# Kernel tuning notes

Hardware: AMD Instinct MI355X
Metric: run time of the kernel (lower is better)

Reference implementation:

```python
import jax, jax.numpy as jnp
import numpy as np

B, S, E, H = 4, 2048, 1024, 16
D = E // H  # head_size = 64


def setup_inputs() -> dict:
    key = jax.random.key(0)
    k1, k2 = jax.random.split(key)
    x = jax.random.normal(k1, (B, S, E), dtype=jnp.float32)
    # fused QKV projection weight (torch Linear(E, 3E, bias=False))
    W_qkv = jax.random.normal(k2, (E, 3 * E), dtype=jnp.float32) * (1.0 / np.sqrt(E))
    return {"x": x, "W_qkv": W_qkv}


def reference(x, W_qkv):
    b, s, e = x.shape
    qkv = x @ W_qkv                              # [B,S,3E]
    q, k, v = jnp.split(qkv, 3, axis=-1)
    # [B,S,E] -> [B,H,S,D]
    q = q.reshape(b, s, H, D).transpose(0, 2, 1, 3)
    k = k.reshape(b, s, H, D).transpose(0, 2, 1, 3)
    v = v.reshape(b, s, H, D).transpose(0, 2, 1, 3)
    scores = jnp.einsum("bhqd,bhkd->bhqk", q, k) * (1.0 / np.sqrt(D))
    causal = jnp.tril(jnp.ones((s, s), dtype=bool))  # [S,S]
    scores = jnp.where(causal[None, None, :, :], scores, jnp.float32(-jnp.inf))
    attn = jax.nn.softmax(scores, axis=-1)
    # dropout is identity in eval mode (p effectively 0 for this baseline)
    out = jnp.einsum("bhqk,bhkd->bhqd", attn, v)  # [B,H,S,D]
    out = out.transpose(0, 2, 1, 3).reshape(b, s, e)
    # NOTE: original forward never applies output_projection; faithful omission.
    return out
```

## Files before the change

kernel.cpp:

```cpp
#include <hip/hip_runtime.h>
#include <hip/hip_bf16.h>
#include <cstdint>
#include <cstddef>

#define GLOBAL_AS __attribute__((address_space(1)))
#define LDS_AS __attribute__((address_space(3)))

typedef short bf16x8 __attribute__((ext_vector_type(8)));
typedef float f32x4 __attribute__((ext_vector_type(4)));

constexpr int Bq = 4, Sq = 2048, Eq = 1024, Hh = 16;
constexpr int M = Bq * Sq;
constexpr int K = 1024;
constexpr int N = 3 * Eq;

#define SMSC 0.18033688f
#define SMBIAS (-16.0f)

#if __has_builtin(__builtin_amdgcn_exp2f)
#define EXP2F(x) __builtin_amdgcn_exp2f(x)
#else
#define EXP2F(x) exp2f(x)
#endif

static __device__ __forceinline__ unsigned f2bf(float f) {
    union { float f; unsigned u; } v; v.f = f;
    unsigned r = v.u + 0x7fffu + ((v.u >> 16) & 1u);
    return r >> 16;
}

static __device__ __forceinline__ unsigned pk2(float a, float b) {
    union { __hip_bfloat162 h; unsigned u; } c;
    c.h = __float22bfloat162_rn(float2{a, b});
    return c.u;
}

static __device__ __forceinline__ void pl32swap(unsigned& a, unsigned& b) {
    asm("v_permlane32_swap_b32 %0, %1" : "+v"(a), "+v"(b));
}
static __device__ __forceinline__ void pl16swap(unsigned& a, unsigned& b) {
    asm("v_permlane16_swap_b32 %0, %1" : "+v"(a), "+v"(b));
}

__global__ __launch_bounds__(256) void prep(const float* __restrict__ X,
                                            unsigned short* __restrict__ Xb,
                                            const float* __restrict__ W,
                                            unsigned short* __restrict__ Wt) {
    __shared__ unsigned short tile[64 * 72];
    const int t = threadIdx.x;
    const int bx = blockIdx.x;
    if (bx < 4096) {
        size_t i = ((size_t)bx * 256 + t) * 8;
        float4 a = *reinterpret_cast<const float4*>(X + i);
        float4 b = *reinterpret_cast<const float4*>(X + i + 4);
        uint4 o;
        o.x = pk2(a.x, a.y);
        o.y = pk2(a.z, a.w);
        o.z = pk2(b.x, b.y);
        o.w = pk2(b.z, b.w);
        *reinterpret_cast<uint4*>(Xb + i) = o;
        return;
    }
    const int idx = bx - 4096;
    const int n0 = (idx % 48) * 64;
    const int k0 = (idx / 48) * 64;
    #pragma unroll
    for (int p = 0; p < 4; ++p) {
        int c = p * 256 + t;
        int row = c >> 4;
        int c4 = (c & 15) * 4;
        float4 v = *reinterpret_cast<const float4*>(W + (size_t)(k0 + row) * N + n0 + c4);
        *reinterpret_cast<unsigned*>(&tile[row * 72 + c4]) = pk2(v.x, v.y);
        *reinterpret_cast<unsigned*>(&tile[row * 72 + c4 + 2]) = pk2(v.z, v.w);
    }
    __syncthreads();
    #pragma unroll
    for (int p = 0; p < 2; ++p) {
        int c = t + p * 256;
        int n = c & 63;
        int kc = (c >> 6) * 8;
        unsigned v[8];
        #pragma unroll
        for (int j = 0; j < 8; ++j) v[j] = tile[(kc + j) * 72 + n];
        uint4 o;
        o.x = v[0] | (v[1] << 16);
        o.y = v[2] | (v[3] << 16);
        o.z = v[4] | (v[5] << 16);
        o.w = v[6] | (v[7] << 16);
        *reinterpret_cast<uint4*>(Wt + (size_t)(n0 + n) * K + k0 + kc) = o;
    }
}

__global__ __launch_bounds__(512) void gemm_qkv(const unsigned short* __restrict__ A,
                                                const unsigned short* __restrict__ Bt,
                                                unsigned short* __restrict__ C,
                                                unsigned short* __restrict__ Vt) {
    __shared__ unsigned short Al[3][256 * 64];
    __shared__ unsigned short Bl[3][128 * 64];
    const int t = threadIdx.x;
    const int lane = t & 63, w = t >> 6;
    const int wm = w >> 1, wn = w & 1;
    const int lr = lane & 15, quad = lane >> 4;
    const int swz = lr & 7;

    const int bid = (int)blockIdx.x;
    const int sid = (bid & 7) * 96 + (bid >> 3);
    const int nb = sid % 24, mb = sid / 24;
    const int m0 = mb * 256, n0 = nb * 128;

    auto stA = [&](int kt, int s, int p) {
        int c = p * 512 + t;
        int row = c >> 3;
        int lch = (c & 7) ^ (row & 7);
        const unsigned short* g = A + (size_t)(m0 + row) * K + kt * 64 + lch * 8;
        __builtin_amdgcn_global_load_lds((const GLOBAL_AS unsigned int*)g,
                                         (LDS_AS unsigned int*)&Al[s][c * 8], 16, 0, 0);
    };
    auto stB = [&](int kt, int s, int p) {
        int c = p * 512 + t;
        int row = c >> 3;
        int lch = (c & 7) ^ (row & 7);
        const unsigned short* g = Bt + (size_t)(n0 + row) * K + kt * 64 + lch * 8;
        __builtin_amdgcn_global_load_lds((const GLOBAL_AS unsigned int*)g,
                                         (LDS_AS unsigned int*)&Bl[s][c * 8], 16, 0, 0);
    };

    f32x4 acc[4][4] = {};

    stA(0, 0, 0); stA(0, 0, 1); stA(0, 0, 2); stA(0, 0, 3); stB(0, 0, 0); stB(0, 0, 1);
    stA(1, 1, 0); stA(1, 1, 1); stA(1, 1, 2); stA(1, 1, 3); stB(1, 1, 0); stB(1, 1, 1);
    asm volatile("s_waitcnt vmcnt(6)" ::: "memory");
    __builtin_amdgcn_s_barrier();

    int buf = 0;
    for (int kt = 0; kt < 16; ++kt) {
        int sb = buf + 2; if (sb >= 3) sb -= 3;
        const unsigned short* Ab = Al[buf];
        const unsigned short* Bb = Bl[buf];

        bf16x8 a0[4], b0[4];
        {
            const int pch = (quad ^ swz) << 3;
            #pragma unroll
            for (int mt = 0; mt < 4; ++mt)
                a0[mt] = *reinterpret_cast<const bf16x8*>(&Ab[(wm * 64 + mt * 16 + lr) * 64 + pch]);
            #pragma unroll
            for (int nt = 0; nt < 4; ++nt)
                b0[nt] = *reinterpret_cast<const bf16x8*>(&Bb[(wn * 64 + nt * 16 + lr) * 64 + pch]);
        }
        if (kt < 14) { stA(kt + 2, sb, 0); stA(kt + 2, sb, 1); stB(kt + 2, sb, 0); }
        __builtin_amdgcn_s_barrier();
        __builtin_amdgcn_s_setprio(1);
        #pragma unroll
        for (int mt = 0; mt < 4; ++mt)
            #pragma unroll
            for (int nt = 0; nt < 4; ++nt)
                acc[mt][nt] = __builtin_amdgcn_mfma_f32_16x16x32_bf16(a0[mt], b0[nt],
                                                                      acc[mt][nt], 0, 0, 0);
        __builtin_amdgcn_s_setprio(0);
        __builtin_amdgcn_s_barrier();

        bf16x8 a1[4], b1[4];
        {
            const int pch = ((4 + quad) ^ swz) << 3;
            #pragma unroll
            for (int mt = 0; mt < 4; ++mt)
                a1[mt] = *reinterpret_cast<const bf16x8*>(&Ab[(wm * 64 + mt * 16 + lr) * 64 + pch]);
            #pragma unroll
            for (int nt = 0; nt < 4; ++nt)
                b1[nt] = *reinterpret_cast<const bf16x8*>(&Bb[(wn * 64 + nt * 16 + lr) * 64 + pch]);
        }
        if (kt < 14) { stA(kt + 2, sb, 2); stA(kt + 2, sb, 3); stB(kt + 2, sb, 1); }
        __builtin_amdgcn_s_barrier();
        if (kt < 14)       asm volatile("s_waitcnt vmcnt(6)" ::: "memory");
        else if (kt == 14) asm volatile("s_waitcnt vmcnt(0)" ::: "memory");
        __builtin_amdgcn_s_setprio(1);
        #pragma unroll
        for (int mt = 0; mt < 4; ++mt)
            #pragma unroll
            for (int nt = 0; nt < 4; ++nt)
                acc[mt][nt] = __builtin_amdgcn_mfma_f32_16x16x32_bf16(a1[mt], b1[nt],
                                                                      acc[mt][nt], 0, 0, 0);
        __builtin_amdgcn_s_setprio(0);
        __builtin_amdgcn_s_barrier();

        buf = buf + 1 == 3 ? 0 : buf + 1;
    }

    if (n0 < 2 * Eq) {
        #pragma unroll
        for (int mt = 0; mt < 4; ++mt)
            #pragma unroll
            for (int nt = 0; nt < 4; ++nt)
                #pragma unroll
                for (int r = 0; r < 4; ++r) {
                    int row = m0 + wm * 64 + mt * 16 + quad * 4 + r;
                    int col = n0 + wn * 64 + nt * 16 + lr;
                    C[(size_t)row * N + col] = (unsigned short)f2bf(acc[mt][nt][r]);
                }
    } else {
        const int b2 = m0 >> 11;
        const int sbase = (m0 & 2047) + wm * 64;
        #pragma unroll
        for (int mt = 0; mt < 4; ++mt)
            #pragma unroll
            for (int nt = 0; nt < 4; ++nt) {
                int hd = n0 - 2 * Eq + wn * 64 + nt * 16 + lr;
                size_t rowV = (size_t)(b2 * Hh + (hd >> 6)) * 64 + (hd & 63);
                int s = sbase + mt * 16 + quad * 4;
                uint2 val;
                val.x = f2bf(acc[mt][nt][0]) | (f2bf(acc[mt][nt][1]) << 16);
                val.y = f2bf(acc[mt][nt][2]) | (f2bf(acc[mt][nt][3]) << 16);
                *reinterpret_cast<uint2*>(Vt + rowV * Sq + s) = val;
            }
    }
}

__global__ __launch_bounds__(256, 4) void flash_attn(const unsigned short* __restrict__ QKV,
                                                     const unsigned short* __restrict__ Vt,
                                                     float* __restrict__ Out) {
    __shared__ unsigned short Klds[2][32 * 64];
    __shared__ unsigned short Vlds[2][64 * 32];
    const int t = threadIdx.x;
    const int lane = t & 63, w = t >> 6;
    const int lr = lane & 15, quad = lane >> 4;
    const int hb = blockIdx.x;
    const int h = hb & 15, b = hb >> 4;
    const int i = 15 - (int)blockIdx.y;
    const int jmax = 4 * i + 3;
    const int jd = 4 * i + w;
    const int qbase = i * 128 + w * 32;
    const int sw = lr & 7;

    const unsigned short* Kbase = QKV + (size_t)b * Sq * N + Eq + h * 64;
    const unsigned short* Vbase = Vt + (size_t)((b * Hh + h) * 64) * Sq;

    bf16x8 ones;
    #pragma unroll
    for (int z = 0; z < 8; ++z) ones[z] = (short)0x3F80;

    auto stage = [&](int j, int buf) {
        const int kv0 = j * 32;
        {
            int row = t >> 3;
            int lch = (t & 7) ^ (row & 7);
            const unsigned short* gk = Kbase + (size_t)(kv0 + row) * N + lch * 8;
            __builtin_amdgcn_global_load_lds((const GLOBAL_AS unsigned int*)gk,
                                             (LDS_AS unsigned int*)&Klds[buf][t * 8], 16, 0, 0);
        }
        {
            int row = t >> 2;
            int ch = t & 3;
            const unsigned short* gv = Vbase + (size_t)row * Sq + kv0 + ch * 8;
            __builtin_amdgcn_global_load_lds((const GLOBAL_AS unsigned int*)gv,
                                             (LDS_AS unsigned int*)&Vlds[buf][t * 8], 16, 0, 0);
        }
    };

    bf16x8 qf[2][2];
    #pragma unroll
    for (int mt = 0; mt < 2; ++mt)
        #pragma unroll
        for (int ks = 0; ks < 2; ++ks)
            qf[mt][ks] = *reinterpret_cast<const bf16x8*>(
                QKV + (size_t)(b * Sq + qbase + mt * 16 + lr) * N + h * 64 + ks * 32 + quad * 8);

    f32x4 o[2][4] = {};
    f32x4 lsum[2] = {};

    stage(0, 0);
    int cur = 0;
    for (int j = 0; j <= jmax; ++j) {
        __syncthreads();
        if (j < jmax) stage(j + 1, cur ^ 1);

        if (j <= jd) {
            const unsigned short* Kb = Klds[cur];
            const unsigned short* Vb = Vlds[cur];
            const int kv0 = j * 32;

            f32x4 sa[2][2] = {};
            #pragma unroll
            for (int ks = 0; ks < 2; ++ks) {
                const int pch = ((ks * 4 + quad) ^ sw) << 3;
                #pragma unroll
                for (int kt = 0; kt < 2; ++kt) {
                    bf16x8 kf = *reinterpret_cast<const bf16x8*>(&Kb[(kt * 16 + lr) * 64 + pch]);
                    #pragma unroll
                    for (int qt = 0; qt < 2; ++qt)
                        sa[kt][qt] = __builtin_amdgcn_mfma_f32_16x16x32_bf16(kf, qf[qt][ks],
                                                                             sa[kt][qt], 0, 0, 0);
                }
            }

            float p[2][2][4];
            if (j == jd) {
                #pragma unroll
                for (int kt = 0; kt < 2; ++kt)
                    #pragma unroll
                    for (int qt = 0; qt < 2; ++qt)
                        #pragma unroll
                        for (int r = 0; r < 4; ++r) {
                            int kvg = kv0 + kt * 16 + quad * 4 + r;
                            int qg = qbase + qt * 16 + lr;
                            float sc = fmaf(sa[kt][qt][r], SMSC, SMBIAS);
                            sc = (kvg > qg) ? -1e30f : sc;
                            p[kt][qt][r] = EXP2F(sc);
                        }
            } else {
                #pragma unroll
                for (int kt = 0; kt < 2; ++kt)
                    #pragma unroll
                    for (int qt = 0; qt < 2; ++qt)
                        #pragma unroll
                        for (int r = 0; r < 4; ++r)
                            p[kt][qt][r] = EXP2F(fmaf(sa[kt][qt][r], SMSC, SMBIAS));
            }

            bf16x8 af[2];
            #pragma unroll
            for (int qt = 0; qt < 2; ++qt) {
                unsigned w00 = pk2(p[0][qt][0], p[0][qt][1]);
                unsigned w01 = pk2(p[0][qt][2], p[0][qt][3]);
                unsigned w10 = pk2(p[1][qt][0], p[1][qt][1]);
                unsigned w11 = pk2(p[1][qt][2], p[1][qt][3]);
                pl32swap(w00, w10); pl16swap(w00, w10);
                pl32swap(w01, w11); pl16swap(w01, w11);
                union { unsigned u[4]; bf16x8 v; } pa;
                pa.u[0] = w00; pa.u[1] = w01; pa.u[2] = w10; pa.u[3] = w11;
                af[qt] = pa.v;
            }

            #pragma unroll
            for (int dt = 0; dt < 4; ++dt) {
                bf16x8 vf = *reinterpret_cast<const bf16x8*>(&Vb[(dt * 16 + lr) * 32 + quad * 8]);
                #pragma unroll
                for (int qt = 0; qt < 2; ++qt)
                    o[qt][dt] = __builtin_amdgcn_mfma_f32_16x16x32_bf16(af[qt], vf,
                                                                        o[qt][dt], 0, 0, 0);
            }
            #pragma unroll
            for (int qt = 0; qt < 2; ++qt)
                lsum[qt] = __builtin_amdgcn_mfma_f32_16x16x32_bf16(af[qt], ones,
                                                                   lsum[qt], 0, 0, 0);
        }
        cur ^= 1;
    }

    #pragma unroll
    for (int mt = 0; mt < 2; ++mt)
        #pragma unroll
        for (int r = 0; r < 4; ++r) {
            float inv = 1.0f / lsum[mt][r];
            int qg = qbase + mt * 16 + quad * 4 + r;
            #pragma unroll
            for (int dt = 0; dt < 4; ++dt)
                Out[(size_t)(b * Sq + qg) * Eq + h * 64 + dt * 16 + lr] = o[mt][dt][r] * inv;
        }
}

extern "C" void kernel_launch(void* const* d_in, const int* in_sizes, int n_in,
                              void* d_out, int out_size, void* d_ws, size_t ws_size,
                              hipStream_t stream) {
    const float* x  = (const float*)d_in[0];
    const float* Wq = (const float*)d_in[1];
    float* out = (float*)d_out;

    unsigned short* xb  = (unsigned short*)d_ws;
    unsigned short* qkv = xb + (size_t)M * K;
    unsigned short* Wt  = qkv + (size_t)M * N;
    unsigned short* Vt  = Wt + (size_t)N * K;

    prep<<<dim3(4096 + 768), 256, 0, stream>>>(x, xb, Wq, Wt);
    gemm_qkv<<<dim3(768), 512, 0, stream>>>(xb, Wt, qkv, Vt);
    flash_attn<<<dim3(Hh * Bq, 16), 256, 0, stream>>>(qkv, Vt, out);
}
```

Before: 209.1 us.

## Split GEMM k-loop into four quadrant phases and reorder attention tile schedule

```diff
diff --git a/kernel.cpp b/kernel.cpp
--- a/kernel.cpp
+++ b/kernel.cpp
@@ -137,50 +137,89 @@
         int sb = buf + 2; if (sb >= 3) sb -= 3;
         const unsigned short* Ab = Al[buf];
         const unsigned short* Bb = Bl[buf];
-
-        bf16x8 a0[4], b0[4];
-        {
-            const int pch = (quad ^ swz) << 3;
-            #pragma unroll
-            for (int mt = 0; mt < 4; ++mt)
-                a0[mt] = *reinterpret_cast<const bf16x8*>(&Ab[(wm * 64 + mt * 16 + lr) * 64 + pch]);
-            #pragma unroll
-            for (int nt = 0; nt < 4; ++nt)
-                b0[nt] = *reinterpret_cast<const bf16x8*>(&Bb[(wn * 64 + nt * 16 + lr) * 64 + pch]);
-        }
-        if (kt < 14) { stA(kt + 2, sb, 0); stA(kt + 2, sb, 1); stB(kt + 2, sb, 0); }
+        const bool st = (kt < 14);
+
+        bf16x8 a0[2][2], a1[2][2], b0[2][2], b1[2][2];
+
+        #pragma unroll
+        for (int i2 = 0; i2 < 2; ++i2)
+            #pragma unroll
+            for (int ks = 0; ks < 2; ++ks) {
+                const int pch = ((ks * 4 + quad) ^ swz) << 3;
+                a0[i2][ks] = *reinterpret_cast<const bf16x8*>(
+                    &Ab[(wm * 64 + i2 * 16 + lr) * 64 + pch]);
+                b0[i2][ks] = *reinterpret_cast<const bf16x8*>(
+                    &Bb[(wn * 64 + i2 * 16 + lr) * 64 + pch]);
+            }
+        if (st) { stA(kt + 2, sb, 0); stA(kt + 2, sb, 1); }
         __builtin_amdgcn_s_barrier();
         __builtin_amdgcn_s_setprio(1);
         #pragma unroll
-        for (int mt = 0; mt < 4; ++mt)
-            #pragma unroll
-            for (int nt = 0; nt < 4; ++nt)
-                acc[mt][nt] = __builtin_amdgcn_mfma_f32_16x16x32_bf16(a0[mt], b0[nt],
-                                                                      acc[mt][nt], 0, 0, 0);
+        for (int mt = 0; mt < 2; ++mt)
+            #pragma unroll
+            for (int nt = 0; nt < 2; ++nt)
+                #pragma unroll
+                for (int ks = 0; ks < 2; ++ks)
+                    acc[mt][nt] = __builtin_amdgcn_mfma_f32_16x16x32_bf16(
+                        a0[mt][ks], b0[nt][ks], acc[mt][nt], 0, 0, 0);
         __builtin_amdgcn_s_setprio(0);
         __builtin_amdgcn_s_barrier();
 
-        bf16x8 a1[4], b1[4];
-        {
-            const int pch = ((4 + quad) ^ swz) << 3;
-            #pragma unroll
-            for (int mt = 0; mt < 4; ++mt)
-                a1[mt] = *reinterpret_cast<const bf16x8*>(&Ab[(wm * 64 + mt * 16 + lr) * 64 + pch]);
-            #pragma unroll
-            for (int nt = 0; nt < 4; ++nt)
-                b1[nt] = *reinterpret_cast<const bf16x8*>(&Bb[(wn * 64 + nt * 16 + lr) * 64 + pch]);
-        }
-        if (kt < 14) { stA(kt + 2, sb, 2); stA(kt + 2, sb, 3); stB(kt + 2, sb, 1); }
-        __builtin_amdgcn_s_barrier();
+        #pragma unroll
+        for (int i2 = 0; i2 < 2; ++i2)
+            #pragma unroll
+            for (int ks = 0; ks < 2; ++ks) {
+                const int pch = ((ks * 4 + quad) ^ swz) << 3;
+                a1[i2][ks] = *reinterpret_cast<const bf16x8*>(
+                    &Ab[(wm * 64 + (2 + i2) * 16 + lr) * 64 + pch]);
+            }
+        if (st) { stA(kt + 2, sb, 2); stA(kt + 2, sb, 3); }
+        __builtin_amdgcn_s_barrier();
+        __builtin_amdgcn_s_setprio(1);
+        #pragma unroll
+        for (int mt = 0; mt < 2; ++mt)
+            #pragma unroll
+            for (int nt = 0; nt < 2; ++nt)
+                #pragma unroll
+                for (int ks = 0; ks < 2; ++ks)
+                    acc[2 + mt][nt] = __builtin_amdgcn_mfma_f32_16x16x32_bf16(
+                        a1[mt][ks], b0[nt][ks], acc[2 + mt][nt], 0, 0, 0);
+        __builtin_amdgcn_s_setprio(0);
+        __builtin_amdgcn_s_barrier();
+
+        #pragma unroll
+        for (int i2 = 0; i2 < 2; ++i2)
+            #pragma unroll
+            for (int ks = 0; ks < 2; ++ks) {
+                const int pch = ((ks * 4 + quad) ^ swz) << 3;
+                b1[i2][ks] = *reinterpret_cast<const bf16x8*>(
+                    &Bb[(wn * 64 + (2 + i2) * 16 + lr) * 64 + pch]);
+            }
+        if (st) { stB(kt + 2, sb, 0); stB(kt + 2, sb, 1); }
+        __builtin_amdgcn_s_barrier();
+        __builtin_amdgcn_s_setprio(1);
+        #pragma unroll
+        for (int mt = 0; mt < 2; ++mt)
+            #pragma unroll
+            for (int nt = 0; nt < 2; ++nt)
+                #pragma unroll
+                for (int ks = 0; ks < 2; ++ks)
+                    acc[mt][2 + nt] = __builtin_amdgcn_mfma_f32_16x16x32_bf16(
+                        a0[mt][ks], b1[nt][ks], acc[mt][2 + nt], 0, 0, 0);
+        __builtin_amdgcn_s_setprio(0);
+        __builtin_amdgcn_s_barrier();
+
         if (kt < 14)       asm volatile("s_waitcnt vmcnt(6)" ::: "memory");
         else if (kt == 14) asm volatile("s_waitcnt vmcnt(0)" ::: "memory");
         __builtin_amdgcn_s_setprio(1);
         #pragma unroll
-        for (int mt = 0; mt < 4; ++mt)
-            #pragma unroll
-            for (int nt = 0; nt < 4; ++nt)
-                acc[mt][nt] = __builtin_amdgcn_mfma_f32_16x16x32_bf16(a1[mt], b1[nt],
-                                                                      acc[mt][nt], 0, 0, 0);
+        for (int mt = 0; mt < 2; ++mt)
+            #pragma unroll
+            for (int nt = 0; nt < 2; ++nt)
+                #pragma unroll
+                for (int ks = 0; ks < 2; ++ks)
+                    acc[2 + mt][2 + nt] = __builtin_amdgcn_mfma_f32_16x16x32_bf16(
+                        a1[mt][ks], b1[nt][ks], acc[2 + mt][2 + nt], 0, 0, 0);
         __builtin_amdgcn_s_setprio(0);
         __builtin_amdgcn_s_barrier();
 
@@ -226,7 +265,9 @@
     const int lr = lane & 15, quad = lane >> 4;
     const int hb = blockIdx.x;
     const int h = hb & 15, b = hb >> 4;
-    const int i = 15 - (int)blockIdx.y;
+    const int yb = (int)blockIdx.y;
+    const int g = yb >> 2, pq = yb & 3;
+    const int i = (g == 0) ? (15 - pq) : (g == 1) ? (8 + pq) : (g == 2) ? (7 - pq) : pq;
     const int jmax = 4 * i + 3;
     const int jd = 4 * i + w;
     const int qbase = i * 128 + w * 32;
```

Measured after the change: 219.6 us. +5.0%, slower.
